# Optimization experiments

Measured on AMD Instinct MI355X. Metric: run time of the kernel, lower is better.

## Reference

```python
import jax, jax.numpy as jnp
import numpy as np

D_MODEL = 1024
NUM_HEADS = 16
D_K = D_MODEL // NUM_HEADS
D_FF = 4096
LN_EPS = 1e-5


def layer_norm(x, gamma, beta):
    mu = jnp.mean(x, axis=-1, keepdims=True)
    var = jnp.var(x, axis=-1, keepdims=True)
    return (x - mu) * jax.lax.rsqrt(var + LN_EPS) * gamma + beta


def setup_inputs() -> dict:
    key = jax.random.key(0)
    ks = jax.random.split(key, 10)
    s = 0.02
    return {
        "x": jax.random.normal(ks[0], (2, 2048, D_MODEL), dtype=jnp.float32),
        # per-head projections stacked: [H, d_model, d_k] (equivalent to the
        # num_heads separate nn.Linear(d_model, d_k, bias=False) modules)
        "Wq": jax.random.normal(ks[1], (NUM_HEADS, D_MODEL, D_K), dtype=jnp.float32) * s,
        "Wk": jax.random.normal(ks[2], (NUM_HEADS, D_MODEL, D_K), dtype=jnp.float32) * s,
        "Wv": jax.random.normal(ks[3], (NUM_HEADS, D_MODEL, D_K), dtype=jnp.float32) * s,
        "Wo": jax.random.normal(ks[4], (D_MODEL, D_MODEL), dtype=jnp.float32) * s,
        "W1": jax.random.normal(ks[5], (D_MODEL, D_FF), dtype=jnp.float32) * s,
        "b1": jnp.zeros((D_FF,), dtype=jnp.float32),
        "W2": jax.random.normal(ks[6], (D_FF, D_MODEL), dtype=jnp.float32) * s,
        "b2": jnp.zeros((D_MODEL,), dtype=jnp.float32),
        "g1": jnp.ones((D_MODEL,), dtype=jnp.float32),
        "beta1": jnp.zeros((D_MODEL,), dtype=jnp.float32),
        "g2": jnp.ones((D_MODEL,), dtype=jnp.float32),
        "beta2": jnp.zeros((D_MODEL,), dtype=jnp.float32),
    }


def reference(x, Wq, Wk, Wv, Wo, W1, b1, W2, b2, g1, beta1, g2, beta2):
    B, S, D = x.shape
    # ---- pre-LN multi-head self-attention ----
    h = layer_norm(x, g1, beta1)
    # batched QKV projections (equivalent to the per-head Python loop)
    Q = jnp.einsum('bsd,hdk->bhsk', h, Wq)  # [B,H,S,dk]
    K = jnp.einsum('bsd,hdk->bhsk', h, Wk)
    V = jnp.einsum('bsd,hdk->bhsk', h, Wv)
    scores = jnp.einsum('bhqk,bhsk->bhqs', Q, K) / jnp.sqrt(jnp.asarray(D_K, x.dtype))
    weights = jax.nn.softmax(scores, axis=-1)  # [B,H,S,S]
    attn = jnp.einsum('bhqs,bhsk->bhqk', weights, V)  # [B,H,S,dk]
    # concat heads along feature dim (head order preserved)
    concat = attn.transpose(0, 2, 1, 3).reshape(B, S, D)
    x = x + concat @ Wo
    # ---- pre-LN FFN (exact erf GELU, matching nn.GELU default) ----
    h2 = layer_norm(x, g2, beta2)
    ffn = jax.nn.gelu(h2 @ W1 + b1, approximate=False) @ W2 + b2
    return x + ffn
```

## Files before the change

kernel.cpp:

```cpp
#include <hip/hip_runtime.h>
#include <stdint.h>


typedef __attribute__((ext_vector_type(8))) short bf16x8;
typedef __attribute__((ext_vector_type(4))) float f32x4;
typedef __attribute__((ext_vector_type(16))) float f32x16;
typedef __attribute__((ext_vector_type(4))) unsigned short u16x4;
typedef __attribute__((ext_vector_type(4))) unsigned int u32x4;

#define DEV __device__ __forceinline__

static constexpr int DM   = 1024;
static constexpr int DFF  = 4096;
static constexpr int NH   = 16;
static constexpr int DKH  = 64;
static constexpr int SEQ  = 2048;
static constexpr int NBAT = 2;
static constexpr int NTOK = NBAT * SEQ;

DEV unsigned short f2bf(float f) {
  union { float f; unsigned int u; } v; v.f = f;
  unsigned int u = v.u;
  return (unsigned short)((u + 0x7fffu + ((u >> 16) & 1u)) >> 16);
}

DEV void gload_lds16(const unsigned short* g, unsigned short* l) {
  __builtin_amdgcn_global_load_lds(
      (const __attribute__((address_space(1))) unsigned int*)g,
      (__attribute__((address_space(3))) unsigned int*)l, 16, 0, 0);
}

DEV float fast_gelu(float x) {
  const float z = fabsf(x) * 0.70710678118654752f;
  const float t = __builtin_amdgcn_rcpf(1.0f + 0.3275911f * z);
  float p = 1.061405429f;
  p = p * t - 1.453152027f;
  p = p * t + 1.421413741f;
  p = p * t - 0.284496736f;
  p = p * t + 0.254829592f;
  p = p * t;
  float erfv = 1.0f - p * __expf(-z * z);
  erfv = copysignf(erfv, x);
  return 0.5f * x * (1.0f + erfv);
}

__global__ __launch_bounds__(256) void ln_kernel(
    const float* __restrict__ x, const float* __restrict__ g,
    const float* __restrict__ be, unsigned short* __restrict__ out) {
  const int row = blockIdx.x;
  const int t = threadIdx.x;
  const int lane = t & 63, w = t >> 6;
  const float4* xr = (const float4*)(x + (size_t)row * DM);
  float4 v = xr[t];
  float s  = v.x + v.y + v.z + v.w;
  float s2 = v.x * v.x + v.y * v.y + v.z * v.z + v.w * v.w;
#pragma unroll
  for (int off = 32; off; off >>= 1) {
    s  += __shfl_down(s, off);
    s2 += __shfl_down(s2, off);
  }
  __shared__ float rs_[4], rq_[4];
  if (lane == 0) { rs_[w] = s; rq_[w] = s2; }
  __syncthreads();
  float fs = rs_[0] + rs_[1] + rs_[2] + rs_[3];
  float fq = rq_[0] + rq_[1] + rq_[2] + rq_[3];
  float mu = fs * (1.0f / DM);
  float var = fq * (1.0f / DM) - mu * mu;
  float rstd = rsqrtf(var + 1e-5f);
  float4 gv = ((const float4*)g)[t];
  float4 bv = ((const float4*)be)[t];
  u16x4 o;
  o[0] = f2bf((v.x - mu) * rstd * gv.x + bv.x);
  o[1] = f2bf((v.y - mu) * rstd * gv.y + bv.y);
  o[2] = f2bf((v.z - mu) * rstd * gv.z + bv.z);
  o[3] = f2bf((v.w - mu) * rstd * gv.w + bv.w);
  *(u16x4*)(out + (size_t)row * DM + t * 4) = o;
}

__global__ __launch_bounds__(256) void transpose_weights(
    const float* __restrict__ Wq, const float* __restrict__ Wk,
    const float* __restrict__ Wv, const float* __restrict__ Wo,
    const float* __restrict__ W1, const float* __restrict__ W2,
    unsigned short* __restrict__ wqkv_t, unsigned short* __restrict__ wo_t,
    unsigned short* __restrict__ w1_t, unsigned short* __restrict__ w2_t) {
  __shared__ float lds[64][65];
  const int t = blockIdx.x;
  const float* inb; unsigned short* outb; int in_ld, out_ld;
  if (t < 768) {
    const int slice = t >> 4, tin = t & 15;
    const int which = slice >> 4, h = slice & 15;
    const float* W = (which == 0) ? Wq : (which == 1) ? Wk : Wv;
    inb = W + (size_t)((h << 10) + (tin << 6)) * 64;
    in_ld = 64;
    outb = wqkv_t + ((size_t)((which << 10) + (h << 6)) << 10) + (tin << 6);
    out_ld = 1024;
  } else if (t < 1024) {
    const int tt = t - 768, tr = tt >> 4, tc = tt & 15;
    inb = Wo + (size_t)(tc << 6) * 1024 + (tr << 6); in_ld = 1024;
    outb = wo_t + (size_t)(tr << 6) * 1024 + (tc << 6); out_ld = 1024;
  } else if (t < 2048) {
    const int tt = t - 1024, tr = tt >> 4, tc = tt & 15;
    inb = W1 + (size_t)(tc << 6) * 4096 + (tr << 6); in_ld = 4096;
    outb = w1_t + (size_t)(tr << 6) * 1024 + (tc << 6); out_ld = 1024;
  } else {
    const int tt = t - 2048, tr = tt >> 6, tc = tt & 63;
    inb = W2 + (size_t)(tc << 6) * 1024 + (tr << 6); in_ld = 1024;
    outb = w2_t + (size_t)(tr << 6) * 4096 + (tc << 6); out_ld = 4096;
  }
  const int j = threadIdx.x & 63, i0 = threadIdx.x >> 6;
#pragma unroll
  for (int p = 0; p < 16; ++p) {
    const int i = i0 + p * 4;
    lds[j][i] = inb[(size_t)i * in_ld + j];
  }
  __syncthreads();
#pragma unroll
  for (int p = 0; p < 16; ++p) {
    const int r = i0 + p * 4;
    outb[(size_t)r * out_ld + j] = f2bf(lds[r][j]);
  }
}

struct EpiArgs {
  unsigned short* q;
  unsigned short* k;
  unsigned short* vt;
  unsigned short* ob16;
  float* of32;
  float* p0;
  const float* bias;
  const float* resid;
};

template <int EPI>
DEV void epilogue_elem(float v, int row, int col, int N, int bz,
                       const EpiArgs& ep) {
  if constexpr (EPI == 0) {
    const int bb = row >> 11, rr = row & 2047;
    if (col < 1024) {
      const int hh = col >> 6, dk = col & 63;
      const int kk = dk >> 4, h8 = (dk >> 3) & 1, e = dk & 7;
      const int qblk = rr >> 5, l31 = rr & 31;
      ep.q[((size_t)(bb * NH + hh) * 64 + qblk) * 2048 + kk * 512 +
           (h8 * 32 + l31) * 8 + e] = f2bf(v * 0.125f);
    } else if (col < 2048) {
      const int c = col - 1024;
      const int hh = c >> 6, dk = c & 63;
      const int kk = dk >> 4, h8 = (dk >> 3) & 1, e = dk & 7;
      const int kvblk = rr >> 5, l31 = rr & 31;
      ep.k[((size_t)(bb * NH + hh) * 64 + kvblk) * 2048 + kk * 512 +
           (h8 * 32 + l31) * 8 + e] = f2bf(v);
    } else {
      const int c = col - 2048, hh = c >> 6, dd = c & 63;
      const int ssw = (rr & ~12) | ((rr & 4) << 1) | ((rr & 8) >> 1);
      const int t64 = ssw >> 6, w = (ssw >> 4) & 3;
      const int h8 = (ssw >> 3) & 1, e = ssw & 7;
      const int dblk = dd >> 5, l31 = dd & 31;
      ep.vt[(((size_t)(bb * NH + hh) * 32 + t64) * 8 + dblk * 4 + w) * 512 +
            (h8 * 32 + l31) * 8 + e] = f2bf(v);
    }
  } else if constexpr (EPI == 1) {
    const size_t idx = (size_t)row * N + col;
    ep.of32[idx] = v + ep.resid[idx];
  } else if constexpr (EPI == 2) {
    ep.ob16[(size_t)row * N + col] = f2bf(fast_gelu(v + ep.bias[col]));
  } else {
    const size_t idx = (size_t)row * N + col;
    if (bz == 0) ep.p0[idx] = v;
    else ep.of32[idx] = ep.of32[idx] + v + ep.bias[col];
  }
}

template <int EPI>
__global__ __launch_bounds__(256) void gemm_pipe(
    const unsigned short* __restrict__ A, const unsigned short* __restrict__ Bt,
    int N, int Kc, int ldk, EpiArgs ep) {
  __shared__ __align__(16) unsigned short Als[2][128 * 64];
  __shared__ __align__(16) unsigned short Bls[2][128 * 64];
  const int t = threadIdx.x, lane = t & 63, wave = t >> 6;
  const int wm = wave >> 1, wn = wave & 1;
  const int g = lane >> 4, r16 = lane & 15;
  const int nx = gridDim.x;
  const int nwg = nx * gridDim.y;
  int wgid = blockIdx.y * nx + blockIdx.x;
  wgid = (wgid & 7) * (nwg >> 3) + (wgid >> 3);
  const int m0 = (wgid / nx) * 128, n0 = (wgid % nx) * 128;
  const int kbase = blockIdx.z * Kc;

  f32x4 acc[4][4];
  const f32x4 z4 = {0.f, 0.f, 0.f, 0.f};
#pragma unroll
  for (int i = 0; i < 4; ++i)
#pragma unroll
    for (int j = 0; j < 4; ++j) acc[i][j] = z4;

  auto stage = [&](int b, int k0) {
#pragma unroll
    for (int i = 0; i < 4; ++i) {
      const int cb = i * 256 + wave * 64;
      const int c = cb + lane;
      const int row = c >> 3;
      const int sc = ((c & 7) ^ (row & 7)) * 8;
      gload_lds16(A + (size_t)(m0 + row) * ldk + kbase + k0 + sc, &Als[b][cb * 8]);
      gload_lds16(Bt + (size_t)(n0 + row) * ldk + kbase + k0 + sc, &Bls[b][cb * 8]);
    }
  };

  const int NT = Kc >> 6;
  stage(0, 0);
  __syncthreads();
  for (int kt = 0; kt < NT; ++kt) {
    const int cur = kt & 1;
    if (kt + 1 < NT) stage(cur ^ 1, (kt + 1) << 6);
    const int sw = r16 & 7;
    bf16x8 af[2][4], bfr[2][4];
#pragma unroll
    for (int ks = 0; ks < 2; ++ks) {
#pragma unroll
      for (int mt = 0; mt < 4; ++mt)
        af[ks][mt] = *(const bf16x8*)&Als[cur][(wm * 64 + mt * 16 + r16) * 64 +
                                              (((ks << 2) | g) ^ sw) * 8];
#pragma unroll
      for (int nt = 0; nt < 4; ++nt)
        bfr[ks][nt] = *(const bf16x8*)&Bls[cur][(wn * 64 + nt * 16 + r16) * 64 +
                                               (((ks << 2) | g) ^ sw) * 8];
    }
    __builtin_amdgcn_s_setprio(1);
#pragma unroll
    for (int ks = 0; ks < 2; ++ks)
#pragma unroll
      for (int mt = 0; mt < 4; ++mt)
#pragma unroll
        for (int nt = 0; nt < 4; ++nt)
          acc[mt][nt] = __builtin_amdgcn_mfma_f32_16x16x32_bf16(
              af[ks][mt], bfr[ks][nt], acc[mt][nt], 0, 0, 0);
    __builtin_amdgcn_s_setprio(0);
    __syncthreads();
  }
#pragma unroll
  for (int mt = 0; mt < 4; ++mt)
#pragma unroll
    for (int nt = 0; nt < 4; ++nt)
#pragma unroll
      for (int r = 0; r < 4; ++r)
        epilogue_elem<EPI>(acc[mt][nt][r], m0 + wm * 64 + mt * 16 + g * 4 + r,
                           n0 + wn * 64 + nt * 16 + r16, N, blockIdx.z, ep);
}

__global__ __launch_bounds__(256) void reduce_add(const float* __restrict__ p,
                                                  float* __restrict__ out) {
  const int i = blockIdx.x * 256 + threadIdx.x;
  float4 a = ((const float4*)p)[i];
  float4 b = ((float4*)out)[i];
  b.x += a.x; b.y += a.y; b.z += a.z; b.w += a.w;
  ((float4*)out)[i] = b;
}

struct AttnState {
  f32x16 o0, o1;
  float m, lsum;
};

DEV void load_k(const unsigned short* kbase, int s, bf16x8 k0[4], bf16x8 k1[4]) {
  const unsigned short* p = kbase + (size_t)(s >> 5) * 2048;
#pragma unroll
  for (int kk = 0; kk < 4; ++kk) {
    k0[kk] = *(const bf16x8*)(p + kk * 512);
    k1[kk] = *(const bf16x8*)(p + 2048 + kk * 512);
  }
}

DEV void attn_tile(const bf16x8 k0[4], const bf16x8 k1[4],
                   const bf16x8 v0[4], const bf16x8 v1[4],
                   const bf16x8 qf[4], AttnState& st) {
  const f32x16 z16 = {0.f};
  f32x16 pA = z16, pB = z16;
  __builtin_amdgcn_s_setprio(1);
#pragma unroll
  for (int kk = 0; kk < 4; ++kk) {
    pA = __builtin_amdgcn_mfma_f32_32x32x16_bf16(k0[kk], qf[kk], pA, 0, 0, 0);
    pB = __builtin_amdgcn_mfma_f32_32x32x16_bf16(k1[kk], qf[kk], pB, 0, 0, 0);
  }
  __builtin_amdgcn_s_setprio(0);
  float m0 = fmaxf(pA[0], pB[0]), m1 = fmaxf(pA[1], pB[1]);
  float m2 = fmaxf(pA[2], pB[2]), m3 = fmaxf(pA[3], pB[3]);
#pragma unroll
  for (int r = 4; r < 16; r += 4) {
    m0 = fmaxf(m0, fmaxf(pA[r + 0], pB[r + 0]));
    m1 = fmaxf(m1, fmaxf(pA[r + 1], pB[r + 1]));
    m2 = fmaxf(m2, fmaxf(pA[r + 2], pB[r + 2]));
    m3 = fmaxf(m3, fmaxf(pA[r + 3], pB[r + 3]));
  }
  float mx = fmaxf(fmaxf(m0, m1), fmaxf(m2, m3));
  mx = fmaxf(mx, __shfl_xor(mx, 32));
  if (__any(mx > st.m + 8.f)) {
    const float mnew = fmaxf(st.m, mx);
    const float corr = __expf(st.m - mnew);
#pragma unroll
    for (int r = 0; r < 16; ++r) { st.o0[r] *= corr; st.o1[r] *= corr; }
    st.lsum *= corr;
    st.m = mnew;
  }
  float ps = 0.f;
#pragma unroll
  for (int r = 0; r < 16; ++r) {
    pA[r] = __expf(pA[r] - st.m); ps += pA[r];
    pB[r] = __expf(pB[r] - st.m); ps += pB[r];
  }
  ps += __shfl_xor(ps, 32);
  st.lsum += ps;
  bf16x8 pw[4];
#pragma unroll
  for (int w = 0; w < 4; ++w) {
    unsigned int wd0, wd1, wd2, wd3;
    const int e0 = (w & 1) * 8;
    if (w < 2) {
      asm("v_cvt_pk_bf16_f32 %0, %1, %2" : "=v"(wd0) : "v"(pA[e0 + 0]), "v"(pA[e0 + 1]));
      asm("v_cvt_pk_bf16_f32 %0, %1, %2" : "=v"(wd1) : "v"(pA[e0 + 2]), "v"(pA[e0 + 3]));
      asm("v_cvt_pk_bf16_f32 %0, %1, %2" : "=v"(wd2) : "v"(pA[e0 + 4]), "v"(pA[e0 + 5]));
      asm("v_cvt_pk_bf16_f32 %0, %1, %2" : "=v"(wd3) : "v"(pA[e0 + 6]), "v"(pA[e0 + 7]));
    } else {
      asm("v_cvt_pk_bf16_f32 %0, %1, %2" : "=v"(wd0) : "v"(pB[e0 + 0]), "v"(pB[e0 + 1]));
      asm("v_cvt_pk_bf16_f32 %0, %1, %2" : "=v"(wd1) : "v"(pB[e0 + 2]), "v"(pB[e0 + 3]));
      asm("v_cvt_pk_bf16_f32 %0, %1, %2" : "=v"(wd2) : "v"(pB[e0 + 4]), "v"(pB[e0 + 5]));
      asm("v_cvt_pk_bf16_f32 %0, %1, %2" : "=v"(wd3) : "v"(pB[e0 + 6]), "v"(pB[e0 + 7]));
    }
    u32x4 wv = {wd0, wd1, wd2, wd3};
    pw[w] = __builtin_bit_cast(bf16x8, wv);
  }
  __builtin_amdgcn_s_setprio(1);
#pragma unroll
  for (int w = 0; w < 4; ++w) {
    st.o0 = __builtin_amdgcn_mfma_f32_32x32x16_bf16(v0[w], pw[w], st.o0, 0, 0, 0);
    st.o1 = __builtin_amdgcn_mfma_f32_32x32x16_bf16(v1[w], pw[w], st.o1, 0, 0, 0);
  }
  __builtin_amdgcn_s_setprio(0);
}

__global__ __launch_bounds__(256, 2) void attn_kernel(
    const unsigned short* __restrict__ Qc, const unsigned short* __restrict__ Kc,
    const unsigned short* __restrict__ Vt, unsigned short* __restrict__ Oc) {
  const int lane = threadIdx.x & 63, wave = threadIdx.x >> 6;
  const int hi = lane >> 5, l31 = lane & 31;
  const int i = blockIdx.x;
  const int k8 = i & 7, mq = i >> 3;
  const int grp = k8 + 8 * (mq >> 4);
  const int qb = mq & 15;
  const int b = grp >> 4, h = grp & 15;
  const int q0 = qb * 128 + wave * 32;

  const unsigned short* qbp = Qc + ((size_t)grp * 64 + (q0 >> 5)) * 2048 + lane * 8;
  const unsigned short* kbp = Kc + (size_t)grp * 64 * 2048 + lane * 8;
  const unsigned short* vbp = Vt + (size_t)grp * 32 * 4096 + lane * 8;

  bf16x8 qf[4];
#pragma unroll
  for (int kk = 0; kk < 4; ++kk) qf[kk] = *(const bf16x8*)(qbp + kk * 512);

  AttnState st;
#pragma unroll
  for (int r = 0; r < 16; ++r) { st.o0[r] = 0.f; st.o1[r] = 0.f; }
  st.m = -1e30f; st.lsum = 0.f;

  bf16x8 kA0[4], kA1[4], kB0[4], kB1[4];
  load_k(kbp, 0, kA0, kA1);

  for (int s0 = 0; s0 < SEQ; s0 += 128) {
    const unsigned short* vt0 = vbp + (size_t)(s0 >> 6) * 4096;
    bf16x8 v0[4], v1[4];
#pragma unroll
    for (int w = 0; w < 4; ++w) {
      v0[w] = *(const bf16x8*)(vt0 + w * 512);
      v1[w] = *(const bf16x8*)(vt0 + 2048 + w * 512);
    }
    load_k(kbp, s0 + 64, kB0, kB1);
    attn_tile(kA0, kA1, v0, v1, qf, st);
    const unsigned short* vt1 = vbp + (size_t)((s0 + 64) >> 6) * 4096;
#pragma unroll
    for (int w = 0; w < 4; ++w) {
      v0[w] = *(const bf16x8*)(vt1 + w * 512);
      v1[w] = *(const bf16x8*)(vt1 + 2048 + w * 512);
    }
    const int snext = (s0 + 128 < SEQ) ? (s0 + 128) : 0;
    load_k(kbp, snext, kA0, kA1);
    attn_tile(kB0, kB1, v0, v1, qf, st);
  }

  const float inv = 1.0f / st.lsum;
  const size_t rowbase = (size_t)b * SEQ;
  unsigned short* op = Oc + (rowbase + q0 + l31) * DM + h * DKH + hi * 4;
#pragma unroll
  for (int dblk = 0; dblk < 2; ++dblk)
#pragma unroll
    for (int g4 = 0; g4 < 4; ++g4) {
      u16x4 stv;
#pragma unroll
      for (int r = 0; r < 4; ++r) {
        const float v = (dblk ? st.o1[g4 * 4 + r] : st.o0[g4 * 4 + r]) * inv;
        stv[r] = f2bf(v);
      }
      *(u16x4*)(op + dblk * 32 + g4 * 8) = stv;
    }
}

extern "C" void kernel_launch(void* const* d_in, const int* in_sizes, int n_in,
                              void* d_out, int out_size, void* d_ws,
                              size_t ws_size, hipStream_t stream) {
  (void)in_sizes; (void)n_in; (void)out_size; (void)ws_size;
  const float* x   = (const float*)d_in[0];
  const float* Wq  = (const float*)d_in[1];
  const float* Wk  = (const float*)d_in[2];
  const float* Wv  = (const float*)d_in[3];
  const float* Wo  = (const float*)d_in[4];
  const float* W1  = (const float*)d_in[5];
  const float* b1  = (const float*)d_in[6];
  const float* W2  = (const float*)d_in[7];
  const float* b2  = (const float*)d_in[8];
  const float* g1  = (const float*)d_in[9];
  const float* be1 = (const float*)d_in[10];
  const float* g2  = (const float*)d_in[11];
  const float* be2 = (const float*)d_in[12];
  float* out = (float*)d_out;

  char* ws = (char*)d_ws;
  const size_t MB = 1024 * 1024;
  unsigned short* h_buf  = (unsigned short*)(ws + 0 * MB);
  unsigned short* wqkv_t = (unsigned short*)(ws + 8 * MB);
  unsigned short* wo_t   = (unsigned short*)(ws + 14 * MB);
  unsigned short* w1_t   = (unsigned short*)(ws + 16 * MB);
  unsigned short* w2_t   = (unsigned short*)(ws + 24 * MB);
  unsigned short* q_attn = (unsigned short*)(ws + 32 * MB);
  unsigned short* k_attn = (unsigned short*)(ws + 40 * MB);
  unsigned short* v_attn = (unsigned short*)(ws + 48 * MB);
  unsigned short* ffn1   = (unsigned short*)(ws + 32 * MB);
  float*          p0     = (float*)(ws + 0 * MB);

  EpiArgs e0 = {}; e0.q = q_attn; e0.k = k_attn; e0.vt = v_attn;
  EpiArgs e1 = {}; e1.of32 = out; e1.resid = x;
  EpiArgs e2 = {}; e2.ob16 = ffn1; e2.bias = b1;
  EpiArgs e4 = {}; e4.of32 = out; e4.p0 = p0; e4.bias = b2;

  transpose_weights<<<3072, 256, 0, stream>>>(Wq, Wk, Wv, Wo, W1, W2,
                                              wqkv_t, wo_t, w1_t, w2_t);
  ln_kernel<<<NTOK, 256, 0, stream>>>(x, g1, be1, h_buf);
  gemm_pipe<0><<<dim3(3072 / 128, NTOK / 128, 1), 256, 0, stream>>>(
      h_buf, wqkv_t, 3072, DM, DM, e0);
  attn_kernel<<<512, 256, 0, stream>>>(q_attn, k_attn, v_attn, h_buf);
  gemm_pipe<1><<<dim3(DM / 128, NTOK / 128, 1), 256, 0, stream>>>(
      h_buf, wo_t, DM, DM, DM, e1);
  ln_kernel<<<NTOK, 256, 0, stream>>>(out, g2, be2, h_buf);
  gemm_pipe<2><<<dim3(DFF / 128, NTOK / 128, 1), 256, 0, stream>>>(
      h_buf, w1_t, DFF, DM, DM, e2);
  gemm_pipe<4><<<dim3(DM / 128, NTOK / 128, 2), 256, 0, stream>>>(
      ffn1, w2_t, DM, DFF / 2, DFF, e4);
  reduce_add<<<4096, 256, 0, stream>>>(p0, out);
}
```

Baseline: 259.2 us.

## Add 256x256-tile GEMM for QKV and FFN1, use exp2 softmax with folded log2e

Introduces a 512-thread GEMM kernel with 256x256 output tiles and double-buffered LDS, with staging of the next tile split across the MFMA loop. It replaces the 128-tile GEMM for the QKV projection and the first FFN matmul to raise data reuse per tile. Separately, the attention softmax now uses exp2 with log2(e) folded into the Q scaling, and the rescale threshold is adjusted to match. The larger tiles cut the workgroup count (192 and 256 blocks), which may underfill the device, and they raise register and LDS pressure.

```diff
diff --git a/kernel.cpp b/kernel.cpp
--- a/kernel.cpp
+++ b/kernel.cpp
@@ -142,7 +142,7 @@
       const int kk = dk >> 4, h8 = (dk >> 3) & 1, e = dk & 7;
       const int qblk = rr >> 5, l31 = rr & 31;
       ep.q[((size_t)(bb * NH + hh) * 64 + qblk) * 2048 + kk * 512 +
-           (h8 * 32 + l31) * 8 + e] = f2bf(v * 0.125f);
+           (h8 * 32 + l31) * 8 + e] = f2bf(v * 0.18033688011112042f);
     } else if (col < 2048) {
       const int c = col - 1024;
       const int hh = c >> 6, dk = c & 63;
@@ -172,6 +172,109 @@
 }
 
 template <int EPI>
+__global__ __launch_bounds__(512, 2) void gemm_256(
+    const unsigned short* __restrict__ A, const unsigned short* __restrict__ Bt,
+    int N, int K, int ldk, EpiArgs ep) {
+  __shared__ __align__(16) unsigned short Als[2][256 * 64];
+  __shared__ __align__(16) unsigned short Bls[2][256 * 64];
+  const int t = threadIdx.x, lane = t & 63, wave = t >> 6;
+  const int wm = wave >> 2, wn = wave & 3;
+  const int g = lane >> 4, r16 = lane & 15;
+  const int nx = gridDim.x, nwg = nx * gridDim.y;
+  int wgid = blockIdx.y * nx + blockIdx.x;
+  wgid = (wgid & 7) * (nwg >> 3) + (wgid >> 3);
+  const int m0 = (wgid / nx) * 256, n0 = (wgid % nx) * 256;
+
+  f32x4 acc[8][4];
+  const f32x4 z4 = {0.f, 0.f, 0.f, 0.f};
+#pragma unroll
+  for (int i = 0; i < 8; ++i)
+#pragma unroll
+    for (int j = 0; j < 4; ++j) acc[i][j] = z4;
+
+  auto stage_half = [&](int b, int k0, int h) {
+#pragma unroll
+    for (int i = 0; i < 2; ++i) {
+      const int c = i * 512 + t;
+      const int row = c >> 3;
+      const int sc = ((c & 7) ^ (row & 7)) * 8;
+      const int dofs = ((h & 1) << 13) + (i * 512 + (wave << 6)) * 8;
+      if (h < 2)
+        gload_lds16(A + (size_t)(m0 + ((h & 1) << 7) + row) * ldk + k0 + sc,
+                    &Als[b][dofs]);
+      else
+        gload_lds16(Bt + (size_t)(n0 + ((h & 1) << 7) + row) * ldk + k0 + sc,
+                    &Bls[b][dofs]);
+    }
+  };
+
+  const int NT = K >> 6;
+#pragma unroll
+  for (int h = 0; h < 4; ++h) stage_half(0, 0, h);
+
+  for (int kt = 0; kt < NT; ++kt) {
+    const int cur = kt & 1;
+    const bool more = (kt + 1) < NT;
+    const int nk0 = (kt + 1) << 6;
+    __builtin_amdgcn_s_barrier();
+    if (more) {
+      stage_half(cur ^ 1, nk0, 0);
+      stage_half(cur ^ 1, nk0, 1);
+      asm volatile("s_waitcnt vmcnt(4)" ::: "memory");
+    } else {
+      asm volatile("s_waitcnt vmcnt(0)" ::: "memory");
+    }
+    __builtin_amdgcn_s_barrier();
+    __builtin_amdgcn_sched_barrier(0);
+
+    bf16x8 Af[8][2];
+#pragma unroll
+    for (int mf = 0; mf < 8; ++mf) {
+      const int row = (wm << 7) + (mf << 4) + r16;
+#pragma unroll
+      for (int ks = 0; ks < 2; ++ks)
+        Af[mf][ks] = *(const bf16x8*)
+            &Als[cur][row * 64 + ((((ks << 2) | g) ^ (row & 7)) << 3)];
+    }
+#pragma unroll
+    for (int qn = 0; qn < 2; ++qn) {
+      bf16x8 Bf[2][2];
+#pragma unroll
+      for (int ni = 0; ni < 2; ++ni) {
+        const int row = (wn << 6) + (((qn << 1) | ni) << 4) + r16;
+#pragma unroll
+        for (int ks = 0; ks < 2; ++ks)
+          Bf[ni][ks] = *(const bf16x8*)
+              &Bls[cur][row * 64 + ((((ks << 2) | g) ^ (row & 7)) << 3)];
+      }
+      __builtin_amdgcn_s_setprio(1);
+#pragma unroll
+      for (int ks = 0; ks < 2; ++ks)
+#pragma unroll
+        for (int mf = 0; mf < 8; ++mf)
+#pragma unroll
+          for (int ni = 0; ni < 2; ++ni)
+            acc[mf][(qn << 1) | ni] = __builtin_amdgcn_mfma_f32_16x16x32_bf16(
+                Af[mf][ks], Bf[ni][ks], acc[mf][(qn << 1) | ni], 0, 0, 0);
+      __builtin_amdgcn_s_setprio(0);
+      if (qn == 0 && more) {
+        stage_half(cur ^ 1, nk0, 2);
+        stage_half(cur ^ 1, nk0, 3);
+      }
+    }
+  }
+#pragma unroll
+  for (int mf = 0; mf < 8; ++mf)
+#pragma unroll
+    for (int nf = 0; nf < 4; ++nf)
+#pragma unroll
+      for (int r = 0; r < 4; ++r)
+        epilogue_elem<EPI>(acc[mf][nf][r],
+                           m0 + (wm << 7) + (mf << 4) + (g << 2) + r,
+                           n0 + (wn << 6) + (nf << 4) + r16, N, 0, ep);
+}
+
+template <int EPI>
 __global__ __launch_bounds__(256) void gemm_pipe(
     const unsigned short* __restrict__ A, const unsigned short* __restrict__ Bt,
     int N, int Kc, int ldk, EpiArgs ep) {
@@ -293,9 +396,9 @@
   }
   float mx = fmaxf(fmaxf(m0, m1), fmaxf(m2, m3));
   mx = fmaxf(mx, __shfl_xor(mx, 32));
-  if (__any(mx > st.m + 8.f)) {
+  if (__any(mx > st.m + 11.5416f)) {
     const float mnew = fmaxf(st.m, mx);
-    const float corr = __expf(st.m - mnew);
+    const float corr = exp2f(st.m - mnew);
 #pragma unroll
     for (int r = 0; r < 16; ++r) { st.o0[r] *= corr; st.o1[r] *= corr; }
     st.lsum *= corr;
@@ -304,8 +407,8 @@
   float ps = 0.f;
 #pragma unroll
   for (int r = 0; r < 16; ++r) {
-    pA[r] = __expf(pA[r] - st.m); ps += pA[r];
-    pB[r] = __expf(pB[r] - st.m); ps += pB[r];
+    pA[r] = exp2f(pA[r] - st.m); ps += pA[r];
+    pB[r] = exp2f(pB[r] - st.m); ps += pB[r];
   }
   ps += __shfl_xor(ps, 32);
   st.lsum += ps;
@@ -443,13 +546,13 @@
   transpose_weights<<<3072, 256, 0, stream>>>(Wq, Wk, Wv, Wo, W1, W2,
                                               wqkv_t, wo_t, w1_t, w2_t);
   ln_kernel<<<NTOK, 256, 0, stream>>>(x, g1, be1, h_buf);
-  gemm_pipe<0><<<dim3(3072 / 128, NTOK / 128, 1), 256, 0, stream>>>(
+  gemm_256<0><<<dim3(3072 / 256, NTOK / 256), 512, 0, stream>>>(
       h_buf, wqkv_t, 3072, DM, DM, e0);
   attn_kernel<<<512, 256, 0, stream>>>(q_attn, k_attn, v_attn, h_buf);
   gemm_pipe<1><<<dim3(DM / 128, NTOK / 128, 1), 256, 0, stream>>>(
       h_buf, wo_t, DM, DM, DM, e1);
   ln_kernel<<<NTOK, 256, 0, stream>>>(out, g2, be2, h_buf);
-  gemm_pipe<2><<<dim3(DFF / 128, NTOK / 128, 1), 256, 0, stream>>>(
+  gemm_256<2><<<dim3(DFF / 256, NTOK / 256), 512, 0, stream>>>(
       h_buf, w1_t, DFF, DM, DM, e2);
   gemm_pipe<4><<<dim3(DM / 128, NTOK / 128, 2), 256, 0, stream>>>(
       ffn1, w2_t, DM, DFF / 2, DFF, e4);
```

After: 264.7 us. +2.1%, slower.
